# Kernel optimization log

Hardware: AMD Instinct MI355X
Metric: run time of the kernel (lower is better)

Reference implementation:

```python
import jax, jax.numpy as jnp
import numpy as np

DIM = 1024
HEADS = 16
HEAD_DIM = DIM // HEADS  # 64


def get_rope_matrix(seq_len: int, dim: int) -> jnp.ndarray:
    # rope[s, d] = concat(cos(s * inv_freq), sin(s * inv_freq))  -> (seq_len, dim)
    half = dim // 2
    inv_freq = 1.0 / (10000.0 ** (jnp.arange(half, dtype=jnp.float32) / half))
    sinusoid = jnp.arange(seq_len, dtype=jnp.float32)[:, None] * inv_freq[None, :]
    return jnp.concatenate([jnp.cos(sinusoid), jnp.sin(sinusoid)], axis=-1)


def setup_inputs() -> dict:
    key = jax.random.key(0)
    ks = jax.random.split(key, 6)
    B, T, D = 2, 2048, DIM
    scale = 1.0 / np.sqrt(D)
    return {
        "x": jax.random.normal(ks[0], (B, T, D), dtype=jnp.float32),
        "Wq": jax.random.normal(ks[1], (D, D), dtype=jnp.float32) * scale,
        "Wk": jax.random.normal(ks[2], (D, D), dtype=jnp.float32) * scale,
        "Wv": jax.random.normal(ks[3], (D, D), dtype=jnp.float32) * scale,
        "Wo": jax.random.normal(ks[4], (D, D), dtype=jnp.float32) * scale,
        "bo": jax.random.normal(ks[5], (D,), dtype=jnp.float32) * 0.01,
    }


def reference(x, Wq, Wk, Wv, Wo, bo):
    B, T, D = x.shape
    H, hd = HEADS, HEAD_DIM

    # projections -> (B, H, T, hd)
    def split_heads(y):
        return y.reshape(B, T, H, hd).transpose(0, 2, 1, 3)

    q = split_heads(x @ Wq)
    k = split_heads(x @ Wk)
    v = split_heads(x @ Wv)

    rope = get_rope_matrix(T, hd)  # (T, hd)

    # apply_rope(v, rope): einsum('...nd,sd->...ns') contracts head_dim -> (B,H,T,T)
    v_r = jnp.einsum('bhnd,sd->bhns', v, rope)

    scores = jax.nn.softmax(jnp.einsum('bhnd,bhmd->bhnm', q, k) / jnp.sqrt(jnp.float32(hd)), axis=-1)
    out = jnp.einsum('bhnm,bhms->bhns', scores, v_r)  # (B,H,T,T)

    # apply_rope(out, rope.T): out2[...,n,s] = sum_t out[...,n,t] * rope[t,s] -> (B,H,T,hd)
    out = jnp.einsum('bhnt,ts->bhns', out, rope)

    out = out.transpose(0, 2, 1, 3).reshape(B, T, D)
    return out @ Wo + bo
```

## Files before the change

### kernel.cpp

```cpp
#include <hip/hip_runtime.h>
#include <math.h>

#define DIM 1024
#define NH 16
#define HD 64
#define TT 2048
#define NTOK 4096

typedef __bf16 bf8v __attribute__((ext_vector_type(8)));
typedef float f4v __attribute__((ext_vector_type(4)));
typedef unsigned short us8 __attribute__((ext_vector_type(8)));
typedef unsigned short us4 __attribute__((ext_vector_type(4)));

static __device__ __forceinline__ unsigned short f2bf(float f) {
    unsigned int u = __float_as_uint(f);
    u += 0x7FFFu + ((u >> 16) & 1u);
    return (unsigned short)(u >> 16);
}
static __device__ __forceinline__ bf8v ld8(const unsigned short* p) {
    return __builtin_bit_cast(bf8v, *(const us8*)p);
}

__global__ void k_prep(const float* __restrict__ x, unsigned short* __restrict__ xb,
                       const float* __restrict__ Wq, const float* __restrict__ Wk,
                       const float* __restrict__ Wv, unsigned short* __restrict__ wt,
                       float* __restrict__ rope) {
    int tid = threadIdx.x;
    int bb = blockIdx.x;
    if (bb < 4096) {
        int i = bb * 256 + tid;
        float4 v = ((const float4*)x)[i];
        us4 o;
        o[0] = f2bf(v.x); o[1] = f2bf(v.y); o[2] = f2bf(v.z); o[3] = f2bf(v.w);
        *(us4*)&xb[i * 4] = o;
    } else if (bb < 7168) {
        __shared__ float tile[32][33];
        bb -= 4096;
        int z = bb >> 10, rem = bb & 1023;
        int bx = rem & 31, by = rem >> 5;
        const float* W = (z == 0) ? Wq : ((z == 1) ? Wk : Wv);
        int tx = tid & 31, ty = tid >> 5;
        int c0 = bx * 32, k0 = by * 32;
#pragma unroll
        for (int j = 0; j < 4; j++)
            tile[ty + j * 8][tx] = W[(k0 + ty + j * 8) * DIM + c0 + tx];
        __syncthreads();
        unsigned short* out = wt + z * DIM * DIM;
#pragma unroll
        for (int j = 0; j < 4; j++)
            out[(c0 + ty + j * 8) * DIM + k0 + tx] = f2bf(tile[tx][ty + j * 8]);
    } else {
        int i = (bb - 7168) * 256 + tid;
        int s = i >> 6, d = i & 63;
        float inv = exp2f(-(float)(d & 31) * (13.287712379549449f / 32.0f));
        float a = (float)s * inv;
        rope[i] = (d < 32) ? cosf(a) : sinf(a);
    }
}

__global__ void k_R(const float* __restrict__ rope, float* __restrict__ R) {
    __shared__ float red[256];
    int d = blockIdx.x;
    int e = threadIdx.x & 63, sl = threadIdx.x >> 6;
    const float* rp = rope + sl * 512 * 64;
    float acc = 0.f;
    for (int s = 0; s < 512; s++)
        acc += rp[s * 64 + d] * rp[s * 64 + e];
    red[threadIdx.x] = acc;
    __syncthreads();
    if (sl == 0)
        R[d * 64 + e] = (red[e] + red[e + 64]) + (red[e + 128] + red[e + 192]);
}

__global__ void k_wo2(const float* __restrict__ Wo, const float* __restrict__ R,
                      unsigned short* __restrict__ wo2t) {
    __shared__ float Rt[64 * 64];
    int tid = threadIdx.x;
#pragma unroll
    for (int i = 0; i < 16; i++) {
        int idx = tid + i * 256;
        int e = idx >> 6, d = idx & 63;
        Rt[idx] = R[d * 64 + e];
    }
    __syncthreads();
    int j = blockIdx.x;
    float acc[4] = {0.f, 0.f, 0.f, 0.f};
    for (int e = 0; e < 64; e++) {
#pragma unroll
        for (int kk = 0; kk < 4; kk++) {
            int r = tid + kk * 256;
            int h = r >> 6, d = r & 63;
            acc[kk] += Rt[e * 64 + d] * Wo[(h * 64 + e) * DIM + j];
        }
    }
#pragma unroll
    for (int kk = 0; kk < 4; kk++)
        wo2t[j * DIM + tid + kk * 256] = f2bf(acc[kk]);
}

#define BK 32
#define LDA 40

__global__ __launch_bounds__(256, 3) void k_gemm_qkv(const unsigned short* __restrict__ A,
                                                     const unsigned short* __restrict__ Bt,
                                                     unsigned short* __restrict__ qk,
                                                     unsigned short* __restrict__ vt) {
    __shared__ unsigned short As[128 * LDA];
    __shared__ unsigned short Bs[128 * LDA];
    const int K = 1024;
    int tid = threadIdx.x;
    int lane = tid & 63, w = tid >> 6;
    int quad = lane >> 4, l16 = lane & 15;
    int m0 = blockIdx.y * 128, n0 = blockIdx.x * 128;
    int sr = tid >> 1, sc = (tid & 1) * 16;
    const unsigned short* Ag = A + (m0 + sr) * K + sc;
    const unsigned short* Bg = Bt + (n0 + sr) * K + sc;
    int wm = (w >> 1) * 64, wn = (w & 1) * 64;

    us8 a0 = *(const us8*)(Ag);
    us8 a1 = *(const us8*)(Ag + 8);
    us8 b0 = *(const us8*)(Bg);
    us8 b1 = *(const us8*)(Bg + 8);

    f4v acc[4][4] = {};
    for (int k0 = 0; k0 < K; k0 += BK) {
        __syncthreads();
        *(us8*)&As[sr * LDA + sc] = a0;
        *(us8*)&As[sr * LDA + sc + 8] = a1;
        *(us8*)&Bs[sr * LDA + sc] = b0;
        *(us8*)&Bs[sr * LDA + sc + 8] = b1;
        __syncthreads();
        if (k0 + BK < K) {
            a0 = *(const us8*)(Ag + k0 + BK);
            a1 = *(const us8*)(Ag + k0 + BK + 8);
            b0 = *(const us8*)(Bg + k0 + BK);
            b1 = *(const us8*)(Bg + k0 + BK + 8);
        }
        bf8v af[4], bf[4];
#pragma unroll
        for (int mt = 0; mt < 4; mt++)
            af[mt] = ld8(&As[(wm + mt * 16 + l16) * LDA + quad * 8]);
#pragma unroll
        for (int nt = 0; nt < 4; nt++)
            bf[nt] = ld8(&Bs[(wn + nt * 16 + l16) * LDA + quad * 8]);
#pragma unroll
        for (int mt = 0; mt < 4; mt++)
#pragma unroll
            for (int nt = 0; nt < 4; nt++)
                acc[mt][nt] = __builtin_amdgcn_mfma_f32_16x16x32_bf16(af[mt], bf[nt], acc[mt][nt], 0, 0, 0);
    }
#pragma unroll
    for (int mt = 0; mt < 4; mt++) {
#pragma unroll
        for (int nt = 0; nt < 4; nt++) {
            int gc = n0 + wn + nt * 16 + l16;
            int h = (gc >> 6) & 15;
            int d = gc & 63;
            if (gc < 2048) {
                float qs = (gc < 1024) ? 0.18033688011111793f : 1.0f;
                int mtx = gc >> 10;
                unsigned short* base = qk + mtx * (NTOK * DIM);
#pragma unroll
                for (int r = 0; r < 4; r++) {
                    int gm = m0 + wm + mt * 16 + quad * 4 + r;
                    int b = gm >> 11, t = gm & 2047;
                    base[((b * NH + h) * TT + t) * HD + d] = f2bf(acc[mt][nt][r] * qs);
                }
            } else {
                int gm0 = m0 + wm + mt * 16 + quad * 4;
                int b = gm0 >> 11, t = gm0 & 2047;
                us4 ov;
#pragma unroll
                for (int r = 0; r < 4; r++)
                    ov[r] = f2bf(acc[mt][nt][r]);
                *(us4*)&vt[(((b * NH + h) * HD) + d) * TT + t] = ov;
            }
        }
    }
}

__global__ __launch_bounds__(256, 3) void k_gemm_out(const unsigned short* __restrict__ A,
                                                     const unsigned short* __restrict__ Bt,
                                                     const float* __restrict__ bo,
                                                     float* __restrict__ out) {
    __shared__ unsigned short As[128 * LDA];
    __shared__ unsigned short Bs[128 * LDA];
    const int K = 1024;
    int tid = threadIdx.x;
    int lane = tid & 63, w = tid >> 6;
    int quad = lane >> 4, l16 = lane & 15;
    int m0 = blockIdx.y * 128, n0 = blockIdx.x * 128;
    int sr = tid >> 1, sc = (tid & 1) * 16;
    const unsigned short* Ag = A + (m0 + sr) * K + sc;
    const unsigned short* Bg = Bt + (n0 + sr) * K + sc;
    int wm = (w >> 1) * 64, wn = (w & 1) * 64;

    us8 a0 = *(const us8*)(Ag);
    us8 a1 = *(const us8*)(Ag + 8);
    us8 b0 = *(const us8*)(Bg);
    us8 b1 = *(const us8*)(Bg + 8);

    f4v acc[4][4] = {};
    for (int k0 = 0; k0 < K; k0 += BK) {
        __syncthreads();
        *(us8*)&As[sr * LDA + sc] = a0;
        *(us8*)&As[sr * LDA + sc + 8] = a1;
        *(us8*)&Bs[sr * LDA + sc] = b0;
        *(us8*)&Bs[sr * LDA + sc + 8] = b1;
        __syncthreads();
        if (k0 + BK < K) {
            a0 = *(const us8*)(Ag + k0 + BK);
            a1 = *(const us8*)(Ag + k0 + BK + 8);
            b0 = *(const us8*)(Bg + k0 + BK);
            b1 = *(const us8*)(Bg + k0 + BK + 8);
        }
        bf8v af[4], bf[4];
#pragma unroll
        for (int mt = 0; mt < 4; mt++)
            af[mt] = ld8(&As[(wm + mt * 16 + l16) * LDA + quad * 8]);
#pragma unroll
        for (int nt = 0; nt < 4; nt++)
            bf[nt] = ld8(&Bs[(wn + nt * 16 + l16) * LDA + quad * 8]);
#pragma unroll
        for (int mt = 0; mt < 4; mt++)
#pragma unroll
            for (int nt = 0; nt < 4; nt++)
                acc[mt][nt] = __builtin_amdgcn_mfma_f32_16x16x32_bf16(af[mt], bf[nt], acc[mt][nt], 0, 0, 0);
    }
#pragma unroll
    for (int mt = 0; mt < 4; mt++) {
#pragma unroll
        for (int nt = 0; nt < 4; nt++) {
            int gc = n0 + wn + nt * 16 + l16;
            float bias = bo[gc];
#pragma unroll
            for (int r = 0; r < 4; r++) {
                int gm = m0 + wm + mt * 16 + quad * 4 + r;
                out[gm * DIM + gc] = acc[mt][nt][r] + bias;
            }
        }
    }
}

#define LQ 72
__global__ __launch_bounds__(256, 4) void k_flash(const unsigned short* __restrict__ qk,
                                                  const unsigned short* __restrict__ vt,
                                                  unsigned short* __restrict__ attn) {
    __shared__ unsigned short Ks[64 * LQ];
    __shared__ unsigned short Vs[80 * LQ];
    __shared__ unsigned short Ps[128 * LQ];
    int tid = threadIdx.x;
    int lane = tid & 63, w = tid >> 6;
    int quad = lane >> 4, l16 = lane & 15;
    int bh = blockIdx.x & 31, qt = blockIdx.x >> 5;
    const unsigned short* Qg = qk + bh * (TT * HD);
    const unsigned short* Kg = qk + NTOK * DIM + bh * (TT * HD);
    const unsigned short* Vtg = vt + bh * (HD * TT);

    for (int idx = tid; idx < 16 * LQ; idx += 256)
        Vs[64 * LQ + idx] = (idx < LQ) ? (unsigned short)0x3F80 : (unsigned short)0;

    {
        int r = tid >> 1, c0 = (tid & 1) * 32;
        const us8* src = (const us8*)(Qg + (qt * 128 + r) * HD + c0);
#pragma unroll
        for (int i = 0; i < 4; i++)
            *(us8*)&Ps[r * LQ + c0 + i * 8] = src[i];
    }
    bf8v qf[2][2];
#pragma unroll
    for (int g = 0; g < 2; g++)
#pragma unroll
        for (int ks = 0; ks < 2; ks++)
            qf[g][ks] = ld8(&Ps[(w * 32 + g * 16 + l16) * LQ + ks * 32 + quad * 8]);

    int sr = tid >> 2, sc = (tid & 3) * 16;
    const unsigned short* Kgp = Kg + sr * HD + sc;
    const unsigned short* Vgp = Vtg + sr * TT + sc;
    us8 kr0 = *(const us8*)(Kgp);
    us8 kr1 = *(const us8*)(Kgp + 8);
    us8 vr0 = *(const us8*)(Vgp);
    us8 vr1 = *(const us8*)(Vgp + 8);

    f4v oacc[5][2] = {};

    for (int it = 0; it < 32; it++) {
        __syncthreads();
        *(us8*)&Ks[sr * LQ + sc] = kr0;
        *(us8*)&Ks[sr * LQ + sc + 8] = kr1;
        *(us8*)&Vs[sr * LQ + sc] = vr0;
        *(us8*)&Vs[sr * LQ + sc + 8] = vr1;
        __syncthreads();
        if (it < 31) {
            Kgp += 64 * HD;
            Vgp += 64;
            kr0 = *(const us8*)(Kgp);
            kr1 = *(const us8*)(Kgp + 8);
            vr0 = *(const us8*)(Vgp);
            vr1 = *(const us8*)(Vgp + 8);
        }

        f4v sacc[4][2] = {};
#pragma unroll
        for (int ks = 0; ks < 2; ks++) {
            bf8v kf[4];
#pragma unroll
            for (int mt = 0; mt < 4; mt++)
                kf[mt] = ld8(&Ks[(mt * 16 + l16) * LQ + ks * 32 + quad * 8]);
#pragma unroll
            for (int mt = 0; mt < 4; mt++)
#pragma unroll
                for (int g = 0; g < 2; g++)
                    sacc[mt][g] = __builtin_amdgcn_mfma_f32_16x16x32_bf16(kf[mt], qf[g][ks], sacc[mt][g], 0, 0, 0);
        }

#pragma unroll
        for (int g = 0; g < 2; g++) {
#pragma unroll
            for (int mt = 0; mt < 4; mt++) {
                float p0 = __builtin_amdgcn_exp2f(sacc[mt][g][0]);
                float p1 = __builtin_amdgcn_exp2f(sacc[mt][g][1]);
                float p2 = __builtin_amdgcn_exp2f(sacc[mt][g][2]);
                float p3 = __builtin_amdgcn_exp2f(sacc[mt][g][3]);
                unsigned int d0 = __builtin_amdgcn_perm(__float_as_uint(p1), __float_as_uint(p0), 0x07060302u);
                unsigned int d1 = __builtin_amdgcn_perm(__float_as_uint(p3), __float_as_uint(p2), 0x07060302u);
                uint2 pk; pk.x = d0; pk.y = d1;
                *(uint2*)&Ps[(w * 32 + g * 16 + l16) * LQ + mt * 16 + quad * 4] = pk;
            }
        }

#pragma unroll
        for (int ks = 0; ks < 2; ks++) {
            bf8v pf[2];
#pragma unroll
            for (int g = 0; g < 2; g++)
                pf[g] = ld8(&Ps[(w * 32 + g * 16 + l16) * LQ + ks * 32 + quad * 8]);
#pragma unroll
            for (int mtd = 0; mtd < 5; mtd++) {
                bf8v vf = ld8(&Vs[(mtd * 16 + l16) * LQ + ks * 32 + quad * 8]);
#pragma unroll
                for (int g = 0; g < 2; g++)
                    oacc[mtd][g] = __builtin_amdgcn_mfma_f32_16x16x32_bf16(vf, pf[g], oacc[mtd][g], 0, 0, 0);
            }
        }
    }

    int b = bh >> 4, h = bh & 15;
#pragma unroll
    for (int g = 0; g < 2; g++) {
        float ssum = __shfl(oacc[4][g][0], l16);
        float inv = 1.0f / ssum;
        int t = qt * 128 + w * 32 + g * 16 + l16;
        unsigned short* dst = attn + (b * TT + t) * DIM + h * HD;
#pragma unroll
        for (int mtd = 0; mtd < 4; mtd++) {
            us4 ov;
#pragma unroll
            for (int r = 0; r < 4; r++)
                ov[r] = f2bf(oacc[mtd][g][r] * inv);
            *(us4*)&dst[mtd * 16 + quad * 4] = ov;
        }
    }
}

extern "C" void kernel_launch(void* const* d_in, const int* in_sizes, int n_in,
                              void* d_out, int out_size, void* d_ws, size_t ws_size,
                              hipStream_t stream) {
    const float* x  = (const float*)d_in[0];
    const float* Wq = (const float*)d_in[1];
    const float* Wk = (const float*)d_in[2];
    const float* Wv = (const float*)d_in[3];
    const float* Wo = (const float*)d_in[4];
    const float* bo = (const float*)d_in[5];
    float* out = (float*)d_out;
    char* ws = (char*)d_ws;

    unsigned short* Xb    = (unsigned short*)(ws);
    unsigned short* Wqkvt = (unsigned short*)(ws + 8388608);
    unsigned short* QK    = (unsigned short*)(ws + 14680064);
    unsigned short* Vt    = (unsigned short*)(ws + 31457280);
    unsigned short* attn  = (unsigned short*)(ws + 39845888);
    unsigned short* Wo2t  = (unsigned short*)(ws + 48234496);
    float*          rope  = (float*)(ws + 50331648);
    float*          Rm    = (float*)(ws + 50855936);

    hipLaunchKernelGGL(k_prep,     dim3(7680),   dim3(256), 0, stream, x, Xb, Wq, Wk, Wv, Wqkvt, rope);
    hipLaunchKernelGGL(k_R,        dim3(64),     dim3(256), 0, stream, rope, Rm);
    hipLaunchKernelGGL(k_wo2,      dim3(1024),   dim3(256), 0, stream, Wo, Rm, Wo2t);
    hipLaunchKernelGGL(k_gemm_qkv, dim3(24, 32), dim3(256), 0, stream, Xb, Wqkvt, QK, Vt);
    hipLaunchKernelGGL(k_flash,    dim3(512),    dim3(256), 0, stream, QK, Vt, attn);
    hipLaunchKernelGGL(k_gemm_out, dim3(8, 32),  dim3(256), 0, stream, attn, Wo2t, bo, out);
}
```

Baseline: 225.2 us.

## Split flash attention over keys, use direct-to-LDS loads, retile Wo2 prep

The flash kernel now splits the key range in two, which doubles the block count to 1024, and writes unnormalised partial outputs plus row sums. A new combine kernel adds the two partials and normalises them. Both GEMMs switch to global_load_lds with an XOR-swizzled unpadded LDS layout in place of register staging. The Wo2 preparation kernel is retiled to stage Wo and R in shared memory. The attention split adds a kernel launch and extra memory traffic for the partials, and the GEMMs lose their register prefetch overlap because each load is now followed by a barrier.

```diff
diff --git a/kernel.cpp b/kernel.cpp
--- a/kernel.cpp
+++ b/kernel.cpp
@@ -19,6 +19,10 @@
 }
 static __device__ __forceinline__ bf8v ld8(const unsigned short* p) {
     return __builtin_bit_cast(bf8v, *(const us8*)p);
+}
+static __device__ __forceinline__ void gl_lds(const unsigned short* g, unsigned short* l) {
+    __builtin_amdgcn_global_load_lds((const __attribute__((address_space(1))) unsigned int*)(g),
+                                     (__attribute__((address_space(3))) unsigned int*)(l), 16, 0, 0);
 }
 
 __global__ void k_prep(const float* __restrict__ x, unsigned short* __restrict__ xb,
@@ -74,75 +78,67 @@
 
 __global__ void k_wo2(const float* __restrict__ Wo, const float* __restrict__ R,
                       unsigned short* __restrict__ wo2t) {
-    __shared__ float Rt[64 * 64];
+    __shared__ float Ws[64 * 65];
+    __shared__ float Rt[64 * 65];
     int tid = threadIdx.x;
-#pragma unroll
-    for (int i = 0; i < 16; i++) {
-        int idx = tid + i * 256;
-        int e = idx >> 6, d = idx & 63;
-        Rt[idx] = R[d * 64 + e];
+    int h = blockIdx.y, j0 = blockIdx.x * 64;
+    for (int idx = tid; idx < 4096; idx += 256) {
+        int e = idx >> 6, j = idx & 63;
+        Ws[e * 65 + j] = Wo[(h * 64 + e) * DIM + j0 + j];
+        Rt[e * 65 + j] = R[j * 64 + e];
     }
     __syncthreads();
-    int j = blockIdx.x;
-    float acc[4] = {0.f, 0.f, 0.f, 0.f};
+    int d = tid & 63, jb = (tid >> 6) * 16;
+    float acc[16] = {};
     for (int e = 0; e < 64; e++) {
-#pragma unroll
-        for (int kk = 0; kk < 4; kk++) {
-            int r = tid + kk * 256;
-            int h = r >> 6, d = r & 63;
-            acc[kk] += Rt[e * 64 + d] * Wo[(h * 64 + e) * DIM + j];
-        }
-    }
-#pragma unroll
-    for (int kk = 0; kk < 4; kk++)
-        wo2t[j * DIM + tid + kk * 256] = f2bf(acc[kk]);
-}
-
-#define BK 32
-#define LDA 40
+        float r = Rt[e * 65 + d];
+#pragma unroll
+        for (int jj = 0; jj < 16; jj++)
+            acc[jj] += r * Ws[e * 65 + jb + jj];
+    }
+#pragma unroll
+    for (int jj = 0; jj < 16; jj++)
+        wo2t[(j0 + jb + jj) * DIM + h * 64 + d] = f2bf(acc[jj]);
+}
+
 
 __global__ __launch_bounds__(256, 3) void k_gemm_qkv(const unsigned short* __restrict__ A,
                                                      const unsigned short* __restrict__ Bt,
                                                      unsigned short* __restrict__ qk,
                                                      unsigned short* __restrict__ vt) {
-    __shared__ unsigned short As[128 * LDA];
-    __shared__ unsigned short Bs[128 * LDA];
+    __shared__ unsigned short As[128 * 32];
+    __shared__ unsigned short Bs[128 * 32];
     const int K = 1024;
     int tid = threadIdx.x;
     int lane = tid & 63, w = tid >> 6;
     int quad = lane >> 4, l16 = lane & 15;
     int m0 = blockIdx.y * 128, n0 = blockIdx.x * 128;
-    int sr = tid >> 1, sc = (tid & 1) * 16;
-    const unsigned short* Ag = A + (m0 + sr) * K + sc;
-    const unsigned short* Bg = Bt + (n0 + sr) * K + sc;
     int wm = (w >> 1) * 64, wn = (w & 1) * 64;
 
-    us8 a0 = *(const us8*)(Ag);
-    us8 a1 = *(const us8*)(Ag + 8);
-    us8 b0 = *(const us8*)(Bg);
-    us8 b1 = *(const us8*)(Bg + 8);
+    int s0 = tid, s1 = 256 + tid;
+    int r0 = s0 >> 2, cc0 = ((s0 & 3) ^ (r0 & 3)) * 8;
+    int r1 = s1 >> 2, cc1 = ((s1 & 3) ^ (r1 & 3)) * 8;
+    const unsigned short* Ag0 = A + (m0 + r0) * K + cc0;
+    const unsigned short* Ag1 = A + (m0 + r1) * K + cc1;
+    const unsigned short* Bg0 = Bt + (n0 + r0) * K + cc0;
+    const unsigned short* Bg1 = Bt + (n0 + r1) * K + cc1;
+    int qx = quad ^ (l16 & 3);
 
     f4v acc[4][4] = {};
-    for (int k0 = 0; k0 < K; k0 += BK) {
-        __syncthreads();
-        *(us8*)&As[sr * LDA + sc] = a0;
-        *(us8*)&As[sr * LDA + sc + 8] = a1;
-        *(us8*)&Bs[sr * LDA + sc] = b0;
-        *(us8*)&Bs[sr * LDA + sc + 8] = b1;
-        __syncthreads();
-        if (k0 + BK < K) {
-            a0 = *(const us8*)(Ag + k0 + BK);
-            a1 = *(const us8*)(Ag + k0 + BK + 8);
-            b0 = *(const us8*)(Bg + k0 + BK);
-            b1 = *(const us8*)(Bg + k0 + BK + 8);
-        }
+    for (int k0 = 0; k0 < K; k0 += 32) {
+        __syncthreads();
+        gl_lds(Ag0 + k0, &As[s0 * 8]);
+        gl_lds(Ag1 + k0, &As[s1 * 8]);
+        gl_lds(Bg0 + k0, &Bs[s0 * 8]);
+        gl_lds(Bg1 + k0, &Bs[s1 * 8]);
+        __syncthreads();
         bf8v af[4], bf[4];
 #pragma unroll
         for (int mt = 0; mt < 4; mt++)
-            af[mt] = ld8(&As[(wm + mt * 16 + l16) * LDA + quad * 8]);
+            af[mt] = ld8(&As[(wm + mt * 16 + l16) * 32 + qx * 8]);
 #pragma unroll
         for (int nt = 0; nt < 4; nt++)
-            bf[nt] = ld8(&Bs[(wn + nt * 16 + l16) * LDA + quad * 8]);
+            bf[nt] = ld8(&Bs[(wn + nt * 16 + l16) * 32 + qx * 8]);
 #pragma unroll
         for (int mt = 0; mt < 4; mt++)
 #pragma unroll
@@ -183,44 +179,39 @@
                                                      const unsigned short* __restrict__ Bt,
                                                      const float* __restrict__ bo,
                                                      float* __restrict__ out) {
-    __shared__ unsigned short As[128 * LDA];
-    __shared__ unsigned short Bs[128 * LDA];
+    __shared__ unsigned short As[128 * 32];
+    __shared__ unsigned short Bs[128 * 32];
     const int K = 1024;
     int tid = threadIdx.x;
     int lane = tid & 63, w = tid >> 6;
     int quad = lane >> 4, l16 = lane & 15;
     int m0 = blockIdx.y * 128, n0 = blockIdx.x * 128;
-    int sr = tid >> 1, sc = (tid & 1) * 16;
-    const unsigned short* Ag = A + (m0 + sr) * K + sc;
-    const unsigned short* Bg = Bt + (n0 + sr) * K + sc;
     int wm = (w >> 1) * 64, wn = (w & 1) * 64;
 
-    us8 a0 = *(const us8*)(Ag);
-    us8 a1 = *(const us8*)(Ag + 8);
-    us8 b0 = *(const us8*)(Bg);
-    us8 b1 = *(const us8*)(Bg + 8);
+    int s0 = tid, s1 = 256 + tid;
+    int r0 = s0 >> 2, cc0 = ((s0 & 3) ^ (r0 & 3)) * 8;
+    int r1 = s1 >> 2, cc1 = ((s1 & 3) ^ (r1 & 3)) * 8;
+    const unsigned short* Ag0 = A + (m0 + r0) * K + cc0;
+    const unsigned short* Ag1 = A + (m0 + r1) * K + cc1;
+    const unsigned short* Bg0 = Bt + (n0 + r0) * K + cc0;
+    const unsigned short* Bg1 = Bt + (n0 + r1) * K + cc1;
+    int qx = quad ^ (l16 & 3);
 
     f4v acc[4][4] = {};
-    for (int k0 = 0; k0 < K; k0 += BK) {
-        __syncthreads();
-        *(us8*)&As[sr * LDA + sc] = a0;
-        *(us8*)&As[sr * LDA + sc + 8] = a1;
-        *(us8*)&Bs[sr * LDA + sc] = b0;
-        *(us8*)&Bs[sr * LDA + sc + 8] = b1;
-        __syncthreads();
-        if (k0 + BK < K) {
-            a0 = *(const us8*)(Ag + k0 + BK);
-            a1 = *(const us8*)(Ag + k0 + BK + 8);
-            b0 = *(const us8*)(Bg + k0 + BK);
-            b1 = *(const us8*)(Bg + k0 + BK + 8);
-        }
+    for (int k0 = 0; k0 < K; k0 += 32) {
+        __syncthreads();
+        gl_lds(Ag0 + k0, &As[s0 * 8]);
+        gl_lds(Ag1 + k0, &As[s1 * 8]);
+        gl_lds(Bg0 + k0, &Bs[s0 * 8]);
+        gl_lds(Bg1 + k0, &Bs[s1 * 8]);
+        __syncthreads();
         bf8v af[4], bf[4];
 #pragma unroll
         for (int mt = 0; mt < 4; mt++)
-            af[mt] = ld8(&As[(wm + mt * 16 + l16) * LDA + quad * 8]);
+            af[mt] = ld8(&As[(wm + mt * 16 + l16) * 32 + qx * 8]);
 #pragma unroll
         for (int nt = 0; nt < 4; nt++)
-            bf[nt] = ld8(&Bs[(wn + nt * 16 + l16) * LDA + quad * 8]);
+            bf[nt] = ld8(&Bs[(wn + nt * 16 + l16) * 32 + qx * 8]);
 #pragma unroll
         for (int mt = 0; mt < 4; mt++)
 #pragma unroll
@@ -245,14 +236,17 @@
 #define LQ 72
 __global__ __launch_bounds__(256, 4) void k_flash(const unsigned short* __restrict__ qk,
                                                   const unsigned short* __restrict__ vt,
-                                                  unsigned short* __restrict__ attn) {
+                                                  unsigned short* __restrict__ Op,
+                                                  float* __restrict__ Ls) {
     __shared__ unsigned short Ks[64 * LQ];
     __shared__ unsigned short Vs[80 * LQ];
     __shared__ unsigned short Ps[128 * LQ];
     int tid = threadIdx.x;
     int lane = tid & 63, w = tid >> 6;
     int quad = lane >> 4, l16 = lane & 15;
-    int bh = blockIdx.x & 31, qt = blockIdx.x >> 5;
+    int bh = blockIdx.x & 31;
+    int sp = (blockIdx.x >> 5) & 1;
+    int qt = blockIdx.x >> 6;
     const unsigned short* Qg = qk + bh * (TT * HD);
     const unsigned short* Kg = qk + NTOK * DIM + bh * (TT * HD);
     const unsigned short* Vtg = vt + bh * (HD * TT);
@@ -275,8 +269,8 @@
             qf[g][ks] = ld8(&Ps[(w * 32 + g * 16 + l16) * LQ + ks * 32 + quad * 8]);
 
     int sr = tid >> 2, sc = (tid & 3) * 16;
-    const unsigned short* Kgp = Kg + sr * HD + sc;
-    const unsigned short* Vgp = Vtg + sr * TT + sc;
+    const unsigned short* Kgp = Kg + (sp * 1024 + sr) * HD + sc;
+    const unsigned short* Vgp = Vtg + sr * TT + sp * 1024 + sc;
     us8 kr0 = *(const us8*)(Kgp);
     us8 kr1 = *(const us8*)(Kgp + 8);
     us8 vr0 = *(const us8*)(Vgp);
@@ -284,14 +278,14 @@
 
     f4v oacc[5][2] = {};
 
-    for (int it = 0; it < 32; it++) {
+    for (int it = 0; it < 16; it++) {
         __syncthreads();
         *(us8*)&Ks[sr * LQ + sc] = kr0;
         *(us8*)&Ks[sr * LQ + sc + 8] = kr1;
         *(us8*)&Vs[sr * LQ + sc] = vr0;
         *(us8*)&Vs[sr * LQ + sc + 8] = vr1;
         __syncthreads();
-        if (it < 31) {
+        if (it < 15) {
             Kgp += 64 * HD;
             Vgp += 64;
             kr0 = *(const us8*)(Kgp);
@@ -346,21 +340,40 @@
     }
 
     int b = bh >> 4, h = bh & 15;
+    unsigned short* Opd = Op + sp * (NTOK * DIM);
 #pragma unroll
     for (int g = 0; g < 2; g++) {
-        float ssum = __shfl(oacc[4][g][0], l16);
-        float inv = 1.0f / ssum;
         int t = qt * 128 + w * 32 + g * 16 + l16;
-        unsigned short* dst = attn + (b * TT + t) * DIM + h * HD;
+        unsigned short* dst = Opd + (b * TT + t) * DIM + h * HD;
 #pragma unroll
         for (int mtd = 0; mtd < 4; mtd++) {
             us4 ov;
 #pragma unroll
             for (int r = 0; r < 4; r++)
-                ov[r] = f2bf(oacc[mtd][g][r] * inv);
+                ov[r] = f2bf(oacc[mtd][g][r]);
             *(us4*)&dst[mtd * 16 + quad * 4] = ov;
         }
-    }
+        if (quad == 0)
+            Ls[sp * 65536 + bh * 2048 + t] = oacc[4][g][0];
+    }
+}
+
+__global__ void k_comb(const unsigned short* __restrict__ Op, const float* __restrict__ Ls,
+                       unsigned short* __restrict__ attn) {
+    int e = (blockIdx.x * 256 + threadIdx.x) * 8;
+    int h = (e >> 6) & 15, t = (e >> 10) & 2047, b = e >> 21;
+    int bh = b * 16 + h;
+    float inv = 1.0f / (Ls[bh * 2048 + t] + Ls[65536 + bh * 2048 + t]);
+    us8 a = *(const us8*)&Op[e];
+    us8 c = *(const us8*)&Op[NTOK * DIM + e];
+    us8 o;
+#pragma unroll
+    for (int j = 0; j < 8; j++) {
+        float fa = __uint_as_float((unsigned int)a[j] << 16);
+        float fc = __uint_as_float((unsigned int)c[j] << 16);
+        o[j] = f2bf((fa + fc) * inv);
+    }
+    *(us8*)&attn[e] = o;
 }
 
 extern "C" void kernel_launch(void* const* d_in, const int* in_sizes, int n_in,
@@ -377,17 +390,20 @@
 
     unsigned short* Xb    = (unsigned short*)(ws);
     unsigned short* Wqkvt = (unsigned short*)(ws + 8388608);
-    unsigned short* QK    = (unsigned short*)(ws + 14680064);
-    unsigned short* Vt    = (unsigned short*)(ws + 31457280);
-    unsigned short* attn  = (unsigned short*)(ws + 39845888);
-    unsigned short* Wo2t  = (unsigned short*)(ws + 48234496);
-    float*          rope  = (float*)(ws + 50331648);
-    float*          Rm    = (float*)(ws + 50855936);
+    unsigned short* Op    = (unsigned short*)(ws);
+    unsigned short* QK    = (unsigned short*)(ws + 16777216);
+    unsigned short* Vt    = (unsigned short*)(ws + 33554432);
+    unsigned short* attn  = (unsigned short*)(ws + 41943040);
+    unsigned short* Wo2t  = (unsigned short*)(ws + 50331648);
+    float*          rope  = (float*)(ws + 52428800);
+    float*          Rm    = (float*)(ws + 52953088);
+    float*          Ls    = (float*)(ws + 52969472);
 
     hipLaunchKernelGGL(k_prep,     dim3(7680),   dim3(256), 0, stream, x, Xb, Wq, Wk, Wv, Wqkvt, rope);
     hipLaunchKernelGGL(k_R,        dim3(64),     dim3(256), 0, stream, rope, Rm);
-    hipLaunchKernelGGL(k_wo2,      dim3(1024),   dim3(256), 0, stream, Wo, Rm, Wo2t);
+    hipLaunchKernelGGL(k_wo2,      dim3(16, 16), dim3(256), 0, stream, Wo, Rm, Wo2t);
     hipLaunchKernelGGL(k_gemm_qkv, dim3(24, 32), dim3(256), 0, stream, Xb, Wqkvt, QK, Vt);
-    hipLaunchKernelGGL(k_flash,    dim3(512),    dim3(256), 0, stream, QK, Vt, attn);
+    hipLaunchKernelGGL(k_flash,    dim3(1024),   dim3(256), 0, stream, QK, Vt, Op, Ls);
+    hipLaunchKernelGGL(k_comb,     dim3(2048),   dim3(256), 0, stream, Op, Ls, attn);
     hipLaunchKernelGGL(k_gemm_out, dim3(8, 32),  dim3(256), 0, stream, attn, Wo2t, bo, out);
 }
```

Result: faster. 220.4 us (-2.1%).
